# Kernel tuning notes

Hardware: AMD Instinct MI355X
Metric: run time of the kernel (lower is better)

## Reference

```python
import jax, jax.numpy as jnp
import numpy as np

R = 8
EPS = 1e-08
EPSS = 1e-12


def _diff_x(x, r):
    left = x[:, :, r:2 * r + 1]
    middle = x[:, :, 2 * r + 1:] - x[:, :, :-2 * r - 1]
    right = x[:, :, -1:] - x[:, :, -2 * r - 1:-r - 1]
    return jnp.concatenate([left, middle, right], axis=2)


def _diff_y(x, r):
    left = x[:, :, :, r:2 * r + 1]
    middle = x[:, :, :, 2 * r + 1:] - x[:, :, :, :-2 * r - 1]
    right = x[:, :, :, -1:] - x[:, :, :, -2 * r - 1:-r - 1]
    return jnp.concatenate([left, middle, right], axis=3)


def box_filter(x, r):
    # cumsum-based (2r+1)x(2r+1) box sum with clamped borders (matches torch BoxFilter)
    return _diff_y(jnp.cumsum(_diff_x(jnp.cumsum(x, axis=2), r), axis=3), r)


def bilinear_resize(x, H, W):
    # F.interpolate(mode='bilinear', align_corners=True) for NCHW
    n, c, h, w = x.shape
    ys = jnp.linspace(0.0, h - 1.0, H)
    xs = jnp.linspace(0.0, w - 1.0, W)
    y0 = jnp.floor(ys).astype(jnp.int32)
    x0 = jnp.floor(xs).astype(jnp.int32)
    y1 = jnp.minimum(y0 + 1, h - 1)
    x1 = jnp.minimum(x0 + 1, w - 1)
    wy = (ys - y0).astype(x.dtype)[None, None, :, None]
    wx = (xs - x0).astype(x.dtype)[None, None, None, :]
    rows = jnp.take(x, y0, axis=2) * (1.0 - wy) + jnp.take(x, y1, axis=2) * wy
    return jnp.take(rows, x0, axis=3) * (1.0 - wx) + jnp.take(rows, x1, axis=3) * wx


def setup_inputs() -> dict:
    key = jax.random.key(0)
    k1, k2, k3, k4 = jax.random.split(key, 4)
    return {
        "lr_x": jax.random.normal(k1, (4, 3, 256, 256), dtype=jnp.float32),
        "lr_y": jax.random.normal(k2, (4, 3, 256, 256), dtype=jnp.float32),
        "hr_x": jax.random.normal(k3, (4, 3, 1024, 1024), dtype=jnp.float32),
        "l_a": jax.random.uniform(k4, (4, 3, 256, 256), dtype=jnp.float32),
    }


def reference(lr_x, lr_y, hr_x, l_a):
    n, c, h, w = lr_x.shape
    _, _, hh, wh = hr_x.shape
    dt = lr_x.dtype

    N = box_filter(jnp.ones((1, 1, h, w), dtype=dt), R)  # local window counts

    l_a = jnp.abs(l_a) + EPSS
    l_t = l_a / jnp.sum(l_a)

    mean_a = box_filter(l_a) if False else box_filter(l_a, R) / N
    mean_a2xy = box_filter(l_a * l_a * lr_x * lr_y, R) / N
    mean_tax = box_filter(l_t * l_a * lr_x, R) / N
    mean_ay = box_filter(l_a * lr_y, R) / N
    mean_a2x2 = box_filter(l_a * l_a * lr_x * lr_x, R) / N
    mean_ax = box_filter(l_a * lr_x, R) / N

    temp = jnp.abs(mean_a2x2 - N * mean_tax * mean_ax)
    A = (mean_a2xy - N * mean_tax * mean_ay) / (temp + EPS)
    b = (mean_ay - A * mean_ax) / mean_a

    A = box_filter(A, R) / N
    b = box_filter(b, R) / N

    mean_A = bilinear_resize(A, hh, wh)
    mean_b = bilinear_resize(b, hh, wh)
    return (mean_A * hr_x + mean_b).astype(jnp.float32)
```

## Files before the change

kernel.cpp:

```cpp
#include <hip/hip_runtime.h>

#define RAD 8
#define HH 256
#define WW 256
#define NC 12
#define PS (HH*WW)
#define SCALE (255.0f/1023.0f)

#define NR3 36
#define NC3 20
#define SP3 33
#define MP3 21

__device__ __forceinline__ int swz3072(int b) { return (b & 7) * 384 + (b >> 3); }
__device__ __forceinline__ int swz1536(int b) { return (b & 7) * 192 + (b >> 3); }

__device__ __forceinline__ float run17(float x) {
    float s = x + __shfl_up(x, 1, 64);
    s += __shfl_up(s, 2, 64);
    s += __shfl_up(s, 4, 64);
    s += __shfl_up(s, 8, 64);
    s += __shfl_up(x, 16, 64);
    return s;
}

__global__ __launch_bounds__(256) void k_reduce(const float* __restrict__ la,
                                                float* __restrict__ partials) {
    int tid = threadIdx.x;
    __shared__ float ls[4];
    const float4* p4 = (const float4*)la;
    int base = blockIdx.x * 2048 + tid;
    float s = 0.f;
    #pragma unroll
    for (int i = 0; i < 8; i++) {
        float4 v = p4[base + i * 256];
        s += (fabsf(v.x) + 1e-12f) + (fabsf(v.y) + 1e-12f) +
             (fabsf(v.z) + 1e-12f) + (fabsf(v.w) + 1e-12f);
    }
    for (int off = 32; off > 0; off >>= 1) s += __shfl_down(s, off, 64);
    int lane = tid & 63, wid = tid >> 6;
    if (lane == 0) ls[wid] = s;
    __syncthreads();
    if (tid == 0) partials[blockIdx.x] = ls[0] + ls[1] + ls[2] + ls[3];
}

__global__ __launch_bounds__(256) void k_ab(const float* __restrict__ la,
                                            const float* __restrict__ lx,
                                            const float* __restrict__ ly,
                                            const float* __restrict__ partials,
                                            float* __restrict__ HA,
                                            float* __restrict__ HB) {
    int tid = threadIdx.x, lane = tid & 63, wv = tid >> 6;
    int gw = swz1536(blockIdx.x) * 4 + wv;
    int p  = gw >> 9;
    int r  = gw & 511;
    int strip = r >> 6;
    int band  = r & 63;
    int i0 = band << 2;
    int C0 = strip << 5;
    int col = C0 - 16 + lane;
    bool vc = (col >= 0) && (col < WW);
    int colc = min(max(col, 0), WW - 1);
    const float* pa = la + p * PS + colc;
    const float* px = lx + p * PS + colc;
    const float* py = ly + p * PS + colc;

    float psum = partials[lane] + ((lane < 32) ? partials[lane + 64] : 0.0f);
    #pragma unroll
    for (int off = 32; off > 0; off >>= 1) psum += __shfl_xor(psum, off, 64);
    float invS = 1.0f / psum;

    int  cA  = C0 - 24 + lane;
    bool vcA = (cA >= 0) && (cA < WW);
    float cxA = (float)(min(cA + RAD, WW - 1) - max(cA - RAD, 0) + 1);
    int  cM  = C0 - 32 + lane;

    float s0 = 0, s1 = 0, s2 = 0, s3 = 0, s4 = 0, s5 = 0;
    auto accum = [&](int rr, float sg) {
        float va = 0.f, vx = 0.f, vy = 0.f;
        if (vc) { int o = rr * WW; va = pa[o]; vx = px[o]; vy = py[o]; }
        float a  = vc ? (fabsf(va) + 1e-12f) : 0.f;
        float ax = a * vx, ay = a * vy;
        s0 = fmaf(sg, a, s0); s1 = fmaf(sg, ax, s1); s2 = fmaf(sg, ay, s2);
        s3 = fmaf(sg, a * ax, s3); s4 = fmaf(sg, ax * ax, s4); s5 = fmaf(sg, ax * ay, s5);
    };

    #pragma unroll
    for (int d = -8; d <= 8; ++d) {
        int rr = i0 + d;
        if (rr >= 0 && rr < HH) accum(rr, 1.0f);
    }

    float* HApl = HA + p * PS;
    float* HBpl = HB + p * PS;
    #pragma unroll
    for (int k = 0; k < 4; ++k) {
        int m = i0 + k;
        if (k > 0) {
            int ra = m + 8; if (ra < HH) accum(ra, 1.0f);
            int rs = m - 9; if (rs >= 0) accum(rs, -1.0f);
        }
        float h0 = run17(s0), h1 = run17(s1), h2 = run17(s2),
              h3 = run17(s3), h4 = run17(s4), h5 = run17(s5);
        float cy = (float)(min(m + RAD, HH - 1) - max(m - RAD, 0) + 1);
        float Nv = cxA * cy, invN = 1.0f / Nv;
        float m_a = h0 * invN, m_ax = h1 * invN, m_ay = h2 * invN;
        float m_tax = h3 * invN * invS;
        float m_a2x2 = h4 * invN, m_a2xy = h5 * invN;
        float tempv = fabsf(m_a2x2 - Nv * m_tax * m_ax);
        float Avt = (m_a2xy - Nv * m_tax * m_ay) / (tempv + 1e-8f);
        float bvt = (m_ay - Avt * m_ax) / m_a;
        float Av = vcA ? Avt : 0.f;
        float bv = vcA ? bvt : 0.f;
        float HtA = run17(Av), HtB = run17(bv);
        if (lane >= 32) {
            int o = m * WW + cM;
            HApl[o] = HtA;
            HBpl[o] = HtB;
        }
    }
}

__global__ __launch_bounds__(256) void k_tile(const float* __restrict__ HA,
                                              const float* __restrict__ HB,
                                              const float* __restrict__ hrx,
                                              float* __restrict__ out) {
    __shared__ float sHA[NR3 * SP3], sHB[NR3 * SP3];
    __shared__ float mAb[NC3 * MP3], mBb[NC3 * MP3];

    int tid = threadIdx.x;
    int b  = swz3072(blockIdx.x);
    int p  = b >> 8;
    int t  = b & 255;
    int ti = t >> 4, tj = t & 15;
    int I0 = ti << 6, J0 = tj << 6;
    int Lr0 = max(0, (I0 * 255) / 1023 - 1);
    int Lc0 = max(0, (J0 * 255) / 1023 - 1);

    int col4 = tid & 15;
    int rg   = tid >> 4;
    int J4 = (J0 >> 2) + col4;
    int planeHR = p * 262144;
    int hidx0 = planeHR + (I0 + 0 * 16 + rg) * 256 + J4;
    int hidx1 = planeHR + (I0 + 1 * 16 + rg) * 256 + J4;
    int hidx2 = planeHR + (I0 + 2 * 16 + rg) * 256 + J4;
    int hidx3 = planeHR + (I0 + 3 * 16 + rg) * 256 + J4;
    const float4* h4 = (const float4*)hrx;
    float4 hp0 = h4[hidx0], hp1 = h4[hidx1], hp2 = h4[hidx2], hp3 = h4[hidx3];

    const float* HApl = HA + p * PS;
    const float* HBpl = HB + p * PS;
    for (int idx = tid; idx < NR3 * 32; idx += 256) {
        int r = idx >> 5, c = idx & 31;
        int gr = Lr0 - 8 + r, gc = Lc0 + c;
        float av = 0.f, bv = 0.f;
        if (gr >= 0 && gr < HH && gc < WW) {
            int o = gr * WW + gc;
            av = HApl[o]; bv = HBpl[o];
        }
        sHA[r * SP3 + c] = av;
        sHB[r * SP3 + c] = bv;
    }
    __syncthreads();

    for (int job = tid; job < 2 * NC3 * NC3; job += 256) {
        int which = (job >= NC3 * NC3);
        int rest  = which ? job - NC3 * NC3 : job;
        int r = rest / NC3, c = rest - r * NC3;
        const float* sp = (which ? sHB : sHA) + r * SP3 + c;
        float s = 0.f;
        #pragma unroll
        for (int j = 0; j < 17; ++j) s += sp[j * SP3];
        int gj = Lc0 + c, gi = Lr0 + r;
        float cxw = (float)(min(gj + RAD, WW - 1) - max(gj - RAD, 0) + 1);
        float cyw = (float)(min(gi + RAD, HH - 1) - max(gi - RAD, 0) + 1);
        (which ? mBb : mAb)[r * MP3 + c] = s / (cxw * cyw);
    }
    __syncthreads();

    {
        int Jp = J4 << 2;
        int xb = (int)((float)Jp * SCALE);
        int i1 = min(xb + 1, WW - 1), i2 = min(xb + 2, WW - 1);
        int lxb = xb - Lc0, li1 = i1 - Lc0, li2 = i2 - Lc0;
        float wxv[4]; bool hs[4];
        #pragma unroll
        for (int k = 0; k < 4; k++) {
            float xsk = (float)(Jp + k) * SCALE;
            int x0 = (int)xsk;
            wxv[k] = xsk - (float)x0;
            hs[k] = (x0 > xb);
        }
        float4* o4 = (float4*)out;

        #pragma unroll
        for (int it = 0; it < 4; ++it) {
            int row = (it << 4) + rg;
            int I = I0 + row;
            float ysf = (float)I * SCALE;
            int y0 = (int)ysf;
            float wy = ysf - (float)y0;
            int y1 = min(y0 + 1, HH - 1);
            int ly0 = y0 - Lr0, ly1 = y1 - Lr0;
            const float* a0p = mAb + ly0 * MP3;
            const float* a1p = mAb + ly1 * MP3;
            const float* b0p = mBb + ly0 * MP3;
            const float* b1p = mBb + ly1 * MP3;
            float A0a = a0p[lxb], A0b = a0p[li1], A0c = a0p[li2];
            float A1a = a1p[lxb], A1b = a1p[li1], A1c = a1p[li2];
            float B0a = b0p[lxb], B0b = b0p[li1], B0c = b0p[li2];
            float B1a = b1p[lxb], B1b = b1p[li1], B1c = b1p[li2];
            float4 h = (it == 0) ? hp0 : (it == 1) ? hp1 : (it == 2) ? hp2 : hp3;
            int hidx = (it == 0) ? hidx0 : (it == 1) ? hidx1 : (it == 2) ? hidx2 : hidx3;
            float hv[4] = {h.x, h.y, h.z, h.w};
            float ov[4];
            float omwy = 1.0f - wy;
            #pragma unroll
            for (int k = 0; k < 4; k++) {
                bool hb = hs[k];
                float Alo0 = hb ? A0b : A0a, Ahi0 = hb ? A0c : A0b;
                float Alo1 = hb ? A1b : A1a, Ahi1 = hb ? A1c : A1b;
                float Blo0 = hb ? B0b : B0a, Bhi0 = hb ? B0c : B0b;
                float Blo1 = hb ? B1b : B1a, Bhi1 = hb ? B1c : B1b;
                float wx = wxv[k], omwx = 1.0f - wx;
                float Ar0 = Alo0 * omwx + Ahi0 * wx;
                float Ar1 = Alo1 * omwx + Ahi1 * wx;
                float Br0 = Blo0 * omwx + Bhi0 * wx;
                float Br1 = Blo1 * omwx + Bhi1 * wx;
                float Avv = Ar0 * omwy + Ar1 * wy;
                float Bvv = Br0 * omwy + Br1 * wy;
                ov[k] = Avv * hv[k] + Bvv;
            }
            float4 o; o.x = ov[0]; o.y = ov[1]; o.z = ov[2]; o.w = ov[3];
            o4[hidx] = o;
        }
    }
}

extern "C" void kernel_launch(void* const* d_in, const int* in_sizes, int n_in,
                              void* d_out, int out_size, void* d_ws, size_t ws_size,
                              hipStream_t stream) {
    const float* lr_x = (const float*)d_in[0];
    const float* lr_y = (const float*)d_in[1];
    const float* hr_x = (const float*)d_in[2];
    const float* l_a  = (const float*)d_in[3];
    float* out = (float*)d_out;

    float* ws       = (float*)d_ws;
    float* partials = ws;
    float* HA       = ws + 256;
    float* HB       = HA + NC * PS;

    k_reduce<<<96, 256, 0, stream>>>(l_a, partials);
    k_ab    <<<1536, 256, 0, stream>>>(l_a, lr_x, lr_y, partials, HA, HB);
    k_tile  <<<3072, 256, 0, stream>>>(HA, HB, hr_x, out);
}
```

Measured before the change: 136.7 us.

## Fuse reduce, A/b, and tile kernels into one persistent kernel with grid barriers

Merges the three launches into a single 768-block kernel that uses atomic-counter grid barriers: the first waits for the global l_a sum and the second waits for all HA/HB rows before the upsampling phase. Each wave now handles 8 rows instead of 4, and each block processes 4 output tiles in a loop. The goal is to remove launch gaps and overlap the row box sums with the reduction. The cost is a memset, spin-waiting that relies on all 768 blocks being co-resident, and fewer blocks available to hide memory latency.

After: 392.1 us. 187% more time.

```diff
diff --git a/kernel.cpp b/kernel.cpp
--- a/kernel.cpp
+++ b/kernel.cpp
@@ -3,7 +3,7 @@
 #define RAD 8
 #define HH 256
 #define WW 256
-#define NC 12
+#define NCP 12
 #define PS (HH*WW)
 #define SCALE (255.0f/1023.0f)
 
@@ -11,9 +11,9 @@
 #define NC3 20
 #define SP3 33
 #define MP3 21
-
-__device__ __forceinline__ int swz3072(int b) { return (b & 7) * 384 + (b >> 3); }
-__device__ __forceinline__ int swz1536(int b) { return (b & 7) * 192 + (b >> 3); }
+#define NBLK 768
+
+__device__ __forceinline__ int swz768(int b) { return (b & 7) * 96 + (b >> 3); }
 
 __device__ __forceinline__ float run17(float x) {
     float s = x + __shfl_up(x, 1, 64);
@@ -24,39 +24,45 @@
     return s;
 }
 
-__global__ __launch_bounds__(256) void k_reduce(const float* __restrict__ la,
-                                                float* __restrict__ partials) {
-    int tid = threadIdx.x;
+__global__ __launch_bounds__(256, 4) void k_all(const float* __restrict__ la,
+                                                const float* __restrict__ lx,
+                                                const float* __restrict__ ly,
+                                                const float* __restrict__ hrx,
+                                                float* __restrict__ ws,
+                                                float* __restrict__ out) {
+    __shared__ float sHA[NR3 * SP3], sHB[NR3 * SP3];
+    __shared__ float mAb[NC3 * MP3], mBb[NC3 * MP3];
     __shared__ float ls[4];
-    const float4* p4 = (const float4*)la;
-    int base = blockIdx.x * 2048 + tid;
-    float s = 0.f;
-    #pragma unroll
-    for (int i = 0; i < 8; i++) {
-        float4 v = p4[base + i * 256];
-        s += (fabsf(v.x) + 1e-12f) + (fabsf(v.y) + 1e-12f) +
-             (fabsf(v.z) + 1e-12f) + (fabsf(v.w) + 1e-12f);
-    }
-    for (int off = 32; off > 0; off >>= 1) s += __shfl_down(s, off, 64);
-    int lane = tid & 63, wid = tid >> 6;
-    if (lane == 0) ls[wid] = s;
-    __syncthreads();
-    if (tid == 0) partials[blockIdx.x] = ls[0] + ls[1] + ls[2] + ls[3];
-}
-
-__global__ __launch_bounds__(256) void k_ab(const float* __restrict__ la,
-                                            const float* __restrict__ lx,
-                                            const float* __restrict__ ly,
-                                            const float* __restrict__ partials,
-                                            float* __restrict__ HA,
-                                            float* __restrict__ HB) {
+
+    unsigned* ctr1 = (unsigned*)ws;
+    unsigned* ctr2 = ctr1 + 1;
+    float* part = ws + 256;
+    float* HA   = ws + 1024;
+    float* HB   = HA + NCP * PS;
+
     int tid = threadIdx.x, lane = tid & 63, wv = tid >> 6;
-    int gw = swz1536(blockIdx.x) * 4 + wv;
-    int p  = gw >> 9;
-    int r  = gw & 511;
-    int strip = r >> 6;
-    int band  = r & 63;
-    int i0 = band << 2;
+    int bid = swz768(blockIdx.x);
+
+    {
+        const float4* p4 = (const float4*)la;
+        float4 v = p4[bid * 256 + tid];
+        float s = (fabsf(v.x) + 1e-12f) + (fabsf(v.y) + 1e-12f) +
+                  (fabsf(v.z) + 1e-12f) + (fabsf(v.w) + 1e-12f);
+        for (int off = 32; off > 0; off >>= 1) s += __shfl_down(s, off, 64);
+        if (lane == 0) ls[wv] = s;
+        __syncthreads();
+        if (tid == 0) {
+            part[bid] = ls[0] + ls[1] + ls[2] + ls[3];
+            __threadfence();
+            __hip_atomic_fetch_add(ctr1, 1u, __ATOMIC_RELEASE, __HIP_MEMORY_SCOPE_AGENT);
+        }
+    }
+
+    int gw4 = bid * 4 + wv;
+    int p   = gw4 >> 8;
+    int rr_ = gw4 & 255;
+    int strip = rr_ >> 5, band = rr_ & 31;
+    int i0 = band << 3;
     int C0 = strip << 5;
     int col = C0 - 16 + lane;
     bool vc = (col >= 0) && (col < WW);
@@ -64,12 +70,6 @@
     const float* pa = la + p * PS + colc;
     const float* px = lx + p * PS + colc;
     const float* py = ly + p * PS + colc;
-
-    float psum = partials[lane] + ((lane < 32) ? partials[lane + 64] : 0.0f);
-    #pragma unroll
-    for (int off = 32; off > 0; off >>= 1) psum += __shfl_xor(psum, off, 64);
-    float invS = 1.0f / psum;
-
     int  cA  = C0 - 24 + lane;
     bool vcA = (cA >= 0) && (cA < WW);
     float cxA = (float)(min(cA + RAD, WW - 1) - max(cA - RAD, 0) + 1);
@@ -91,10 +91,24 @@
         if (rr >= 0 && rr < HH) accum(rr, 1.0f);
     }
 
+    {
+        int guard = 0;
+        while (__hip_atomic_load(ctr1, __ATOMIC_ACQUIRE, __HIP_MEMORY_SCOPE_AGENT) < NBLK) {
+            __builtin_amdgcn_s_sleep(32);
+            if (++guard > (1 << 20)) break;
+        }
+    }
+    float psum = 0.f;
+    #pragma unroll
+    for (int j = 0; j < 12; ++j) psum += part[lane + 64 * j];
+    #pragma unroll
+    for (int off = 32; off > 0; off >>= 1) psum += __shfl_xor(psum, off, 64);
+    float invS = 1.0f / psum;
+
     float* HApl = HA + p * PS;
     float* HBpl = HB + p * PS;
     #pragma unroll
-    for (int k = 0; k < 4; ++k) {
+    for (int k = 0; k < 8; ++k) {
         int m = i0 + k;
         if (k > 0) {
             int ra = m + 8; if (ra < HH) accum(ra, 1.0f);
@@ -119,121 +133,127 @@
             HBpl[o] = HtB;
         }
     }
-}
-
-__global__ __launch_bounds__(256) void k_tile(const float* __restrict__ HA,
-                                              const float* __restrict__ HB,
-                                              const float* __restrict__ hrx,
-                                              float* __restrict__ out) {
-    __shared__ float sHA[NR3 * SP3], sHB[NR3 * SP3];
-    __shared__ float mAb[NC3 * MP3], mBb[NC3 * MP3];
-
-    int tid = threadIdx.x;
-    int b  = swz3072(blockIdx.x);
-    int p  = b >> 8;
-    int t  = b & 255;
-    int ti = t >> 4, tj = t & 15;
-    int I0 = ti << 6, J0 = tj << 6;
-    int Lr0 = max(0, (I0 * 255) / 1023 - 1);
-    int Lc0 = max(0, (J0 * 255) / 1023 - 1);
-
-    int col4 = tid & 15;
-    int rg   = tid >> 4;
-    int J4 = (J0 >> 2) + col4;
-    int planeHR = p * 262144;
-    int hidx0 = planeHR + (I0 + 0 * 16 + rg) * 256 + J4;
-    int hidx1 = planeHR + (I0 + 1 * 16 + rg) * 256 + J4;
-    int hidx2 = planeHR + (I0 + 2 * 16 + rg) * 256 + J4;
-    int hidx3 = planeHR + (I0 + 3 * 16 + rg) * 256 + J4;
+
+    __threadfence();
+    __syncthreads();
+    if (tid == 0) {
+        __hip_atomic_fetch_add(ctr2, 1u, __ATOMIC_RELEASE, __HIP_MEMORY_SCOPE_AGENT);
+        int guard = 0;
+        while (__hip_atomic_load(ctr2, __ATOMIC_ACQUIRE, __HIP_MEMORY_SCOPE_AGENT) < NBLK) {
+            __builtin_amdgcn_s_sleep(32);
+            if (++guard > (1 << 20)) break;
+        }
+    }
+    __syncthreads();
+    __threadfence();
+
     const float4* h4 = (const float4*)hrx;
-    float4 hp0 = h4[hidx0], hp1 = h4[hidx1], hp2 = h4[hidx2], hp3 = h4[hidx3];
-
-    const float* HApl = HA + p * PS;
-    const float* HBpl = HB + p * PS;
-    for (int idx = tid; idx < NR3 * 32; idx += 256) {
-        int r = idx >> 5, c = idx & 31;
-        int gr = Lr0 - 8 + r, gc = Lc0 + c;
-        float av = 0.f, bv = 0.f;
-        if (gr >= 0 && gr < HH && gc < WW) {
-            int o = gr * WW + gc;
-            av = HApl[o]; bv = HBpl[o];
-        }
-        sHA[r * SP3 + c] = av;
-        sHB[r * SP3 + c] = bv;
-    }
-    __syncthreads();
-
-    for (int job = tid; job < 2 * NC3 * NC3; job += 256) {
-        int which = (job >= NC3 * NC3);
-        int rest  = which ? job - NC3 * NC3 : job;
-        int r = rest / NC3, c = rest - r * NC3;
-        const float* sp = (which ? sHB : sHA) + r * SP3 + c;
-        float s = 0.f;
-        #pragma unroll
-        for (int j = 0; j < 17; ++j) s += sp[j * SP3];
-        int gj = Lc0 + c, gi = Lr0 + r;
-        float cxw = (float)(min(gj + RAD, WW - 1) - max(gj - RAD, 0) + 1);
-        float cyw = (float)(min(gi + RAD, HH - 1) - max(gi - RAD, 0) + 1);
-        (which ? mBb : mAb)[r * MP3 + c] = s / (cxw * cyw);
-    }
-    __syncthreads();
-
-    {
-        int Jp = J4 << 2;
-        int xb = (int)((float)Jp * SCALE);
-        int i1 = min(xb + 1, WW - 1), i2 = min(xb + 2, WW - 1);
-        int lxb = xb - Lc0, li1 = i1 - Lc0, li2 = i2 - Lc0;
-        float wxv[4]; bool hs[4];
-        #pragma unroll
-        for (int k = 0; k < 4; k++) {
-            float xsk = (float)(Jp + k) * SCALE;
-            int x0 = (int)xsk;
-            wxv[k] = xsk - (float)x0;
-            hs[k] = (x0 > xb);
-        }
-        float4* o4 = (float4*)out;
-
-        #pragma unroll
-        for (int it = 0; it < 4; ++it) {
-            int row = (it << 4) + rg;
-            int I = I0 + row;
-            float ysf = (float)I * SCALE;
-            int y0 = (int)ysf;
-            float wy = ysf - (float)y0;
-            int y1 = min(y0 + 1, HH - 1);
-            int ly0 = y0 - Lr0, ly1 = y1 - Lr0;
-            const float* a0p = mAb + ly0 * MP3;
-            const float* a1p = mAb + ly1 * MP3;
-            const float* b0p = mBb + ly0 * MP3;
-            const float* b1p = mBb + ly1 * MP3;
-            float A0a = a0p[lxb], A0b = a0p[li1], A0c = a0p[li2];
-            float A1a = a1p[lxb], A1b = a1p[li1], A1c = a1p[li2];
-            float B0a = b0p[lxb], B0b = b0p[li1], B0c = b0p[li2];
-            float B1a = b1p[lxb], B1b = b1p[li1], B1c = b1p[li2];
-            float4 h = (it == 0) ? hp0 : (it == 1) ? hp1 : (it == 2) ? hp2 : hp3;
-            int hidx = (it == 0) ? hidx0 : (it == 1) ? hidx1 : (it == 2) ? hidx2 : hidx3;
-            float hv[4] = {h.x, h.y, h.z, h.w};
-            float ov[4];
-            float omwy = 1.0f - wy;
+    float4* o4 = (float4*)out;
+    for (int tt = 0; tt < 4; ++tt) {
+        int b  = bid * 4 + tt;
+        int tp = b >> 8;
+        int t  = b & 255;
+        int ti = t >> 4, tj = t & 15;
+        int I0 = ti << 6, J0 = tj << 6;
+        int Lr0 = max(0, (I0 * 255) / 1023 - 1);
+        int Lc0 = max(0, (J0 * 255) / 1023 - 1);
+
+        int col4 = tid & 15;
+        int rg   = tid >> 4;
+        int J4 = (J0 >> 2) + col4;
+        int planeHR = tp * 262144;
+        int hidx0 = planeHR + (I0 + 0 * 16 + rg) * 256 + J4;
+        int hidx1 = planeHR + (I0 + 1 * 16 + rg) * 256 + J4;
+        int hidx2 = planeHR + (I0 + 2 * 16 + rg) * 256 + J4;
+        int hidx3 = planeHR + (I0 + 3 * 16 + rg) * 256 + J4;
+        float4 hp0 = h4[hidx0], hp1 = h4[hidx1], hp2 = h4[hidx2], hp3 = h4[hidx3];
+
+        const float* HAq = HA + tp * PS;
+        const float* HBq = HB + tp * PS;
+        for (int idx = tid; idx < NR3 * 32; idx += 256) {
+            int r = idx >> 5, c = idx & 31;
+            int gr = Lr0 - 8 + r, gc = Lc0 + c;
+            float av = 0.f, bv = 0.f;
+            if (gr >= 0 && gr < HH && gc < WW) {
+                int o = gr * WW + gc;
+                av = HAq[o]; bv = HBq[o];
+            }
+            sHA[r * SP3 + c] = av;
+            sHB[r * SP3 + c] = bv;
+        }
+        __syncthreads();
+
+        for (int job = tid; job < 2 * NC3 * NC3; job += 256) {
+            int which = (job >= NC3 * NC3);
+            int rest  = which ? job - NC3 * NC3 : job;
+            int r = rest / NC3, c = rest - r * NC3;
+            const float* sp = (which ? sHB : sHA) + r * SP3 + c;
+            float s = 0.f;
+            #pragma unroll
+            for (int j = 0; j < 17; ++j) s += sp[j * SP3];
+            int gj = Lc0 + c, gi = Lr0 + r;
+            float cxw = (float)(min(gj + RAD, WW - 1) - max(gj - RAD, 0) + 1);
+            float cyw = (float)(min(gi + RAD, HH - 1) - max(gi - RAD, 0) + 1);
+            (which ? mBb : mAb)[r * MP3 + c] = s / (cxw * cyw);
+        }
+        __syncthreads();
+
+        {
+            int Jp = J4 << 2;
+            int xb = (int)((float)Jp * SCALE);
+            int i1 = min(xb + 1, WW - 1), i2 = min(xb + 2, WW - 1);
+            int lxb = xb - Lc0, li1 = i1 - Lc0, li2 = i2 - Lc0;
+            float wxv[4]; bool hs[4];
             #pragma unroll
             for (int k = 0; k < 4; k++) {
-                bool hb = hs[k];
-                float Alo0 = hb ? A0b : A0a, Ahi0 = hb ? A0c : A0b;
-                float Alo1 = hb ? A1b : A1a, Ahi1 = hb ? A1c : A1b;
-                float Blo0 = hb ? B0b : B0a, Bhi0 = hb ? B0c : B0b;
-                float Blo1 = hb ? B1b : B1a, Bhi1 = hb ? B1c : B1b;
-                float wx = wxv[k], omwx = 1.0f - wx;
-                float Ar0 = Alo0 * omwx + Ahi0 * wx;
-                float Ar1 = Alo1 * omwx + Ahi1 * wx;
-                float Br0 = Blo0 * omwx + Bhi0 * wx;
-                float Br1 = Blo1 * omwx + Bhi1 * wx;
-                float Avv = Ar0 * omwy + Ar1 * wy;
-                float Bvv = Br0 * omwy + Br1 * wy;
-                ov[k] = Avv * hv[k] + Bvv;
+                float xsk = (float)(Jp + k) * SCALE;
+                int x0 = (int)xsk;
+                wxv[k] = xsk - (float)x0;
+                hs[k] = (x0 > xb);
             }
-            float4 o; o.x = ov[0]; o.y = ov[1]; o.z = ov[2]; o.w = ov[3];
-            o4[hidx] = o;
-        }
+            #pragma unroll
+            for (int it = 0; it < 4; ++it) {
+                int row = (it << 4) + rg;
+                int I = I0 + row;
+                float ysf = (float)I * SCALE;
+                int y0 = (int)ysf;
+                float wy = ysf - (float)y0;
+                int y1 = min(y0 + 1, HH - 1);
+                int ly0 = y0 - Lr0, ly1 = y1 - Lr0;
+                const float* a0p = mAb + ly0 * MP3;
+                const float* a1p = mAb + ly1 * MP3;
+                const float* b0p = mBb + ly0 * MP3;
+                const float* b1p = mBb + ly1 * MP3;
+                float A0a = a0p[lxb], A0b = a0p[li1], A0c = a0p[li2];
+                float A1a = a1p[lxb], A1b = a1p[li1], A1c = a1p[li2];
+                float B0a = b0p[lxb], B0b = b0p[li1], B0c = b0p[li2];
+                float B1a = b1p[lxb], B1b = b1p[li1], B1c = b1p[li2];
+                float4 h = (it == 0) ? hp0 : (it == 1) ? hp1 : (it == 2) ? hp2 : hp3;
+                int hidx = (it == 0) ? hidx0 : (it == 1) ? hidx1 : (it == 2) ? hidx2 : hidx3;
+                float hv[4] = {h.x, h.y, h.z, h.w};
+                float ov[4];
+                float omwy = 1.0f - wy;
+                #pragma unroll
+                for (int k = 0; k < 4; k++) {
+                    bool hb = hs[k];
+                    float Alo0 = hb ? A0b : A0a, Ahi0 = hb ? A0c : A0b;
+                    float Alo1 = hb ? A1b : A1a, Ahi1 = hb ? A1c : A1b;
+                    float Blo0 = hb ? B0b : B0a, Bhi0 = hb ? B0c : B0b;
+                    float Blo1 = hb ? B1b : B1a, Bhi1 = hb ? B1c : B1b;
+                    float wx = wxv[k], omwx = 1.0f - wx;
+                    float Ar0 = Alo0 * omwx + Ahi0 * wx;
+                    float Ar1 = Alo1 * omwx + Ahi1 * wx;
+                    float Br0 = Blo0 * omwx + Bhi0 * wx;
+                    float Br1 = Blo1 * omwx + Bhi1 * wx;
+                    float Avv = Ar0 * omwy + Ar1 * wy;
+                    float Bvv = Br0 * omwy + Br1 * wy;
+                    ov[k] = Avv * hv[k] + Bvv;
+                }
+                float4 o; o.x = ov[0]; o.y = ov[1]; o.z = ov[2]; o.w = ov[3];
+                o4[hidx] = o;
+            }
+        }
+        __syncthreads();
     }
 }
 
@@ -245,13 +265,8 @@
     const float* hr_x = (const float*)d_in[2];
     const float* l_a  = (const float*)d_in[3];
     float* out = (float*)d_out;
-
-    float* ws       = (float*)d_ws;
-    float* partials = ws;
-    float* HA       = ws + 256;
-    float* HB       = HA + NC * PS;
-
-    k_reduce<<<96, 256, 0, stream>>>(l_a, partials);
-    k_ab    <<<1536, 256, 0, stream>>>(l_a, lr_x, lr_y, partials, HA, HB);
-    k_tile  <<<3072, 256, 0, stream>>>(HA, HB, hr_x, out);
+    float* ws  = (float*)d_ws;
+
+    hipMemsetAsync(d_ws, 0, 4096, stream);
+    k_all<<<NBLK, 256, 0, stream>>>(l_a, lr_x, lr_y, hr_x, ws, out);
 }
```
